# Optimization experiments

Hardware: AMD Instinct MI355X
Metric: run time of the kernel (lower is better)

Reference implementation:

```python
import jax, jax.numpy as jnp
import numpy as np

B, L, HC, D = 4, 4096, 4, 1024
K, DIL = 4, 2
EPS = 1e-5
C = HC * D
PAD = (K - 1) * DIL


def setup_inputs() -> dict:
    key = jax.random.key(0)
    k1, k2, k3 = jax.random.split(key, 3)
    x = jax.random.normal(k1, (B, L, HC, D), dtype=jnp.float32)
    # RMSNorm affine weights, one per chunk (torch init: ones; randomize slightly for a
    # non-trivial baseline)
    norm_weight = 1.0 + 0.02 * jax.random.normal(k2, (HC, D), dtype=jnp.float32)
    # depthwise conv weight [C, 1, K] (torch init is zeros; use small random values so
    # the kernel-correctness baseline is non-degenerate)
    conv_weight = 0.1 * jax.random.normal(k3, (C, 1, K), dtype=jnp.float32)
    return {"x": x, "norm_weight": norm_weight, "conv_weight": conv_weight}


def reference(x, norm_weight, conv_weight):
    # per-chunk RMSNorm over last dim: [B, L, HC, D]
    ms = jnp.mean(jnp.square(x), axis=-1, keepdims=True)
    xn = x * jax.lax.rsqrt(ms + EPS) * norm_weight[None, None, :, :]
    # concat chunks along feature dim -> [B, L, C], then to [B, C, L]
    xc = xn.reshape(B, L, C).transpose(0, 2, 1)
    # depthwise dilated causal conv1d: left-pad (K-1)*DIL, output length L
    y = jax.lax.conv_general_dilated(
        xc, conv_weight,
        window_strides=(1,),
        padding=((PAD, 0),),
        rhs_dilation=(DIL,),
        feature_group_count=C,
        dimension_numbers=("NCH", "OIH", "NCH"),
    )
    y = jax.nn.silu(y)
    # back to [B, L, HC, D]
    return y.transpose(0, 2, 1).reshape(B, L, HC, D)
```

## Files before the change

kernel.cpp:

```cpp
#include <hip/hip_runtime.h>

namespace {

constexpr int B = 4, L = 4096, HC = 4, D = 1024, K = 4, DIL = 2;
constexpr int PAD = (K - 1) * DIL;
constexpr float EPS = 1e-5f;
constexpr int CL = 64;
constexpr int ST = 8;
constexpr int NSTEP = CL / ST;
constexpr int NT = L / CL;
constexpr int BDIM = 256;

typedef float f32x4 __attribute__((ext_vector_type(4)));

#define LGKM_BARRIER() do {                                    \
    asm volatile("s_waitcnt lgkmcnt(0)" ::: "memory");         \
    __builtin_amdgcn_s_barrier();                              \
} while (0)

__device__ __forceinline__ void stage16(const float* g, float* l) {
    __builtin_amdgcn_global_load_lds(
        (const __attribute__((address_space(1))) void*)g,
        (__attribute__((address_space(3))) void*)l, 16, 0, 0);
}

__global__ __launch_bounds__(BDIM, 2) void engram_shortconv_ldspipe(
    const float* __restrict__ x,
    const float* __restrict__ nw,
    const float* __restrict__ cw,
    float* __restrict__ out)
{
    __shared__ float s_buf[2][ST][BDIM * 4];
    __shared__ float s_part[ST][BDIM];
    __shared__ float s_inv[ST];

    const int blk = blockIdx.x;
    const int t   = blk % NT;
    const int hc  = (blk / NT) % HC;
    const int b   = blk / (NT * HC);
    const int l0  = t * CL;

    const int tid  = threadIdx.x;
    const int wave = tid >> 6;
    const int lane = tid & 63;

    const size_t rs = (size_t)HC * D;
    const float* xcol = x   + ((size_t)b * L * HC + (size_t)hc) * D + tid * 4;
    float*       ocol = out + ((size_t)b * L * HC + (size_t)hc) * D + tid * 4;

    const float4 nw4 = *(const float4*)(nw + (size_t)hc * D + tid * 4);
    float4 cwv[4];
    #pragma unroll
    for (int j = 0; j < 4; ++j)
        cwv[j] = *(const float4*)(cw + ((size_t)hc * D + tid * 4 + j) * K);

    float win[PAD][4];
    if (l0 >= PAD) {
        #pragma unroll
        for (int r = 0; r < PAD; ++r) {
            const float4 v = *(const float4*)(xcol + (size_t)(l0 - PAD + r) * rs);
            win[r][0] = v.x; win[r][1] = v.y; win[r][2] = v.z; win[r][3] = v.w;
        }
    } else {
        #pragma unroll
        for (int r = 0; r < PAD; ++r) {
            const int l = l0 - PAD + r;
            float4 v = make_float4(0.f, 0.f, 0.f, 0.f);
            if (l >= 0) v = *(const float4*)(xcol + (size_t)l * rs);
            win[r][0] = v.x; win[r][1] = v.y; win[r][2] = v.z; win[r][3] = v.w;
        }
    }

    #pragma unroll
    for (int r = 0; r < ST; ++r)
        stage16(xcol + (size_t)(l0 + r) * rs, &s_buf[0][r][wave * 256]);
    #pragma unroll
    for (int r = 0; r < ST; ++r)
        stage16(xcol + (size_t)(l0 + ST + r) * rs, &s_buf[1][r][wave * 256]);

    float wk[4][4];
    {
        const float gv[4] = { nw4.x, nw4.y, nw4.z, nw4.w };
        #pragma unroll
        for (int j = 0; j < 4; ++j) {
            wk[j][0] = cwv[j].x * gv[j]; wk[j][1] = cwv[j].y * gv[j];
            wk[j][2] = cwv[j].z * gv[j]; wk[j][3] = cwv[j].w * gv[j];
        }
    }

    #pragma unroll
    for (int r = 0; r < PAD; ++r)
        s_part[r][tid] = win[r][0]*win[r][0] + win[r][1]*win[r][1]
                       + win[r][2]*win[r][2] + win[r][3]*win[r][3];
    LGKM_BARRIER();
    {
        int rr = wave;
        float s1 = s_part[rr][lane]       + s_part[rr][lane + 64]
                 + s_part[rr][lane + 128] + s_part[rr][lane + 192];
        #pragma unroll
        for (int off = 32; off >= 1; off >>= 1) s1 += __shfl_xor(s1, off);
        if (lane == 0) s_inv[rr] = rsqrtf(s1 * (1.0f / D) + EPS);
        rr = wave + 4;
        if (rr < PAD) {
            float s2 = s_part[rr][lane]       + s_part[rr][lane + 64]
                     + s_part[rr][lane + 128] + s_part[rr][lane + 192];
            #pragma unroll
            for (int off = 32; off >= 1; off >>= 1) s2 += __shfl_xor(s2, off);
            if (lane == 0) s_inv[rr] = rsqrtf(s2 * (1.0f / D) + EPS);
        }
    }
    LGKM_BARRIER();
    #pragma unroll
    for (int r = 0; r < PAD; ++r) {
        const float iv = s_inv[r];
        win[r][0] *= iv; win[r][1] *= iv; win[r][2] *= iv; win[r][3] *= iv;
    }

    #pragma unroll
    for (int s = 0; s < NSTEP; ++s) {
        const int cb = s & 1;

        if (s == 0)                 asm volatile("s_waitcnt vmcnt(8)"  ::: "memory");
        else if (s == 1)            asm volatile("s_waitcnt vmcnt(16)" ::: "memory");
        else if (s == NSTEP - 1)    asm volatile("s_waitcnt vmcnt(16)" ::: "memory");
        else                        asm volatile("s_waitcnt vmcnt(24)" ::: "memory");
        __builtin_amdgcn_sched_barrier(0);

        float cur[ST][4];
        #pragma unroll
        for (int r = 0; r < ST; ++r) {
            const f32x4 v = *(const f32x4*)&s_buf[cb][r][tid * 4];
            cur[r][0] = v.x; cur[r][1] = v.y; cur[r][2] = v.z; cur[r][3] = v.w;
        }
        #pragma unroll
        for (int r = 0; r < ST; ++r)
            s_part[r][tid] = cur[r][0]*cur[r][0] + cur[r][1]*cur[r][1]
                           + cur[r][2]*cur[r][2] + cur[r][3]*cur[r][3];

        if (s < NSTEP - 2) {
            asm volatile("s_waitcnt lgkmcnt(0)" ::: "memory");
            __builtin_amdgcn_sched_barrier(0);
            #pragma unroll
            for (int r = 0; r < ST; ++r)
                stage16(xcol + (size_t)(l0 + (s + 2) * ST + r) * rs,
                        &s_buf[cb][r][wave * 256]);
            __builtin_amdgcn_sched_barrier(0);
        }

        LGKM_BARRIER();
        {
            int rr = wave;
            float s1 = s_part[rr][lane]       + s_part[rr][lane + 64]
                     + s_part[rr][lane + 128] + s_part[rr][lane + 192];
            #pragma unroll
            for (int off = 32; off >= 1; off >>= 1) s1 += __shfl_xor(s1, off);
            if (lane == 0) s_inv[rr] = rsqrtf(s1 * (1.0f / D) + EPS);
            rr = wave + 4;
            float s2 = s_part[rr][lane]       + s_part[rr][lane + 64]
                     + s_part[rr][lane + 128] + s_part[rr][lane + 192];
            #pragma unroll
            for (int off = 32; off >= 1; off >>= 1) s2 += __shfl_xor(s2, off);
            if (lane == 0) s_inv[rr] = rsqrtf(s2 * (1.0f / D) + EPS);
        }
        LGKM_BARRIER();

        const int base = l0 + s * ST;
        #pragma unroll
        for (int r = 0; r < ST; ++r) {
            const float iv = s_inv[r];
            cur[r][0] *= iv; cur[r][1] *= iv; cur[r][2] *= iv; cur[r][3] *= iv;
        }

        #pragma unroll
        for (int i = 0; i < ST; ++i) {
            float av[4];
            #pragma unroll
            for (int j = 0; j < 4; ++j) {
                float a = 0.0f;
                #pragma unroll
                for (int k = 0; k < 4; ++k) {
                    const int rel = i - 6 + 2 * k;
                    const float xv = (rel < 0) ? win[6 + rel][j] : cur[rel][j];
                    a = fmaf(wk[j][k], xv, a);
                }
                av[j] = a / (1.0f + __expf(-a));
            }
            f32x4 o = { av[0], av[1], av[2], av[3] };
            *(f32x4*)(ocol + (size_t)(base + i) * rs) = o;
        }

        #pragma unroll
        for (int r = 0; r < PAD; ++r) {
            win[r][0] = cur[r + 2][0]; win[r][1] = cur[r + 2][1];
            win[r][2] = cur[r + 2][2]; win[r][3] = cur[r + 2][3];
        }
    }
}

}

extern "C" void kernel_launch(void* const* d_in, const int* in_sizes, int n_in,
                              void* d_out, int out_size, void* d_ws, size_t ws_size,
                              hipStream_t stream) {
    const float* x  = (const float*)d_in[0];
    const float* nw = (const float*)d_in[1];
    const float* cw = (const float*)d_in[2];
    float* out = (float*)d_out;

    const int nblocks = B * HC * NT;
    engram_shortconv_ldspipe<<<dim3(nblocks), dim3(BDIM), 0, stream>>>(x, nw, cw, out);
}
```

Measured before the change: 111.7 us.

## Triple-buffer LDS staging and compute row norms one step ahead

Switches from a double-buffered 8-row stage to a triple-buffered 4-row stage pipeline. Each wave now computes one row's RMS directly from LDS one step ahead, which removes the s_part partial-sum buffer and one barrier per step. The halo rows' norms are computed from global loads, and occupancy is raised to 4 blocks per CU. The blockIdx is also remapped to interleave tiles across XCDs. The cost is more loop iterations and more prefetch bookkeeping, with tighter vmcnt waits.

Result: no change. 111.8 us (+0.1%).

```diff
diff --git a/kernel.cpp b/kernel.cpp
--- a/kernel.cpp
+++ b/kernel.cpp
@@ -2,12 +2,12 @@
 
 namespace {
 
-constexpr int B = 4, L = 4096, HC = 4, D = 1024, K = 4, DIL = 2;
-constexpr int PAD = (K - 1) * DIL;
+constexpr int NB = 4, L = 4096, HC = 4, D = 1024, KW = 4;
+constexpr int PAD = 6;
 constexpr float EPS = 1e-5f;
-constexpr int CL = 64;
-constexpr int ST = 8;
-constexpr int NSTEP = CL / ST;
+constexpr int ST = 4;
+constexpr int NSTEP = 16;
+constexpr int CL = ST * NSTEP;
 constexpr int NT = L / CL;
 constexpr int BDIM = 256;
 
@@ -24,59 +24,68 @@
         (__attribute__((address_space(3))) void*)l, 16, 0, 0);
 }
 
-__global__ __launch_bounds__(BDIM, 2) void engram_shortconv_ldspipe(
+__global__ __launch_bounds__(BDIM, 4) void engram_shortconv_tri(
     const float* __restrict__ x,
     const float* __restrict__ nw,
     const float* __restrict__ cw,
     float* __restrict__ out)
 {
-    __shared__ float s_buf[2][ST][BDIM * 4];
-    __shared__ float s_part[ST][BDIM];
-    __shared__ float s_inv[ST];
-
-    const int blk = blockIdx.x;
-    const int t   = blk % NT;
-    const int hc  = (blk / NT) % HC;
-    const int b   = blk / (NT * HC);
-    const int l0  = t * CL;
+    __shared__ float s_buf[3][ST][D];
+    __shared__ float s_inv[2][ST];
+    __shared__ float s_invh[PAD];
+
+    const int lblk = (blockIdx.x & 7) * 128 + (blockIdx.x >> 3);
+    const int t    = lblk % NT;
+    const int hc   = (lblk / NT) % HC;
+    const int b    = lblk / (NT * HC);
+    const int l0   = t * CL;
 
     const int tid  = threadIdx.x;
     const int wave = tid >> 6;
     const int lane = tid & 63;
 
     const size_t rs = (size_t)HC * D;
-    const float* xcol = x   + ((size_t)b * L * HC + (size_t)hc) * D + tid * 4;
-    float*       ocol = out + ((size_t)b * L * HC + (size_t)hc) * D + tid * 4;
+    const float* xbase = x + ((size_t)b * L * HC + (size_t)hc) * D;
+    const float* xcol  = xbase + tid * 4;
+    float*       ocol  = out + ((size_t)b * L * HC + (size_t)hc) * D + tid * 4;
+
+    #pragma unroll
+    for (int s = 0; s < 3; ++s)
+        #pragma unroll
+        for (int r = 0; r < ST; ++r)
+            stage16(xcol + (size_t)(l0 + s * ST + r) * rs, &s_buf[s][r][wave * 256]);
 
     const float4 nw4 = *(const float4*)(nw + (size_t)hc * D + tid * 4);
     float4 cwv[4];
     #pragma unroll
     for (int j = 0; j < 4; ++j)
-        cwv[j] = *(const float4*)(cw + ((size_t)hc * D + tid * 4 + j) * K);
+        cwv[j] = *(const float4*)(cw + ((size_t)hc * D + tid * 4 + j) * KW);
 
     float win[PAD][4];
-    if (l0 >= PAD) {
-        #pragma unroll
-        for (int r = 0; r < PAD; ++r) {
-            const float4 v = *(const float4*)(xcol + (size_t)(l0 - PAD + r) * rs);
-            win[r][0] = v.x; win[r][1] = v.y; win[r][2] = v.z; win[r][3] = v.w;
-        }
-    } else {
-        #pragma unroll
-        for (int r = 0; r < PAD; ++r) {
-            const int l = l0 - PAD + r;
-            float4 v = make_float4(0.f, 0.f, 0.f, 0.f);
-            if (l >= 0) v = *(const float4*)(xcol + (size_t)l * rs);
-            win[r][0] = v.x; win[r][1] = v.y; win[r][2] = v.z; win[r][3] = v.w;
-        }
-    }
-
-    #pragma unroll
-    for (int r = 0; r < ST; ++r)
-        stage16(xcol + (size_t)(l0 + r) * rs, &s_buf[0][r][wave * 256]);
-    #pragma unroll
-    for (int r = 0; r < ST; ++r)
-        stage16(xcol + (size_t)(l0 + ST + r) * rs, &s_buf[1][r][wave * 256]);
+    #pragma unroll
+    for (int r = 0; r < PAD; ++r) {
+        const int l = l0 - PAD + r;
+        float4 v = make_float4(0.f, 0.f, 0.f, 0.f);
+        if (l >= 0) v = *(const float4*)(xcol + (size_t)l * rs);
+        win[r][0] = v.x; win[r][1] = v.y; win[r][2] = v.z; win[r][3] = v.w;
+    }
+
+    #pragma unroll
+    for (int rr = wave; rr < PAD; rr += 4) {
+        const int l = l0 - PAD + rr;
+        float ss = 0.0f;
+        if (l >= 0) {
+            const float* rp = xbase + (size_t)l * rs;
+            #pragma unroll
+            for (int q = 0; q < 4; ++q) {
+                const f32x4 v = *(const f32x4*)(rp + lane * 4 + q * 256);
+                ss = fmaf(v.x, v.x, fmaf(v.y, v.y, fmaf(v.z, v.z, fmaf(v.w, v.w, ss))));
+            }
+        }
+        #pragma unroll
+        for (int off = 32; off >= 1; off >>= 1) ss += __shfl_xor(ss, off);
+        if (lane == 0) s_invh[rr] = rsqrtf(ss * (1.0f / D) + EPS);
+    }
 
     float wk[4][4];
     {
@@ -88,89 +97,53 @@
         }
     }
 
-    #pragma unroll
-    for (int r = 0; r < PAD; ++r)
-        s_part[r][tid] = win[r][0]*win[r][0] + win[r][1]*win[r][1]
-                       + win[r][2]*win[r][2] + win[r][3]*win[r][3];
     LGKM_BARRIER();
+    #pragma unroll
+    for (int r = 0; r < PAD; ++r) {
+        const float iv = s_invh[r];
+        win[r][0] *= iv; win[r][1] *= iv; win[r][2] *= iv; win[r][3] *= iv;
+    }
+    asm volatile("s_waitcnt vmcnt(0)" ::: "memory");
+    __builtin_amdgcn_s_barrier();
     {
-        int rr = wave;
-        float s1 = s_part[rr][lane]       + s_part[rr][lane + 64]
-                 + s_part[rr][lane + 128] + s_part[rr][lane + 192];
-        #pragma unroll
-        for (int off = 32; off >= 1; off >>= 1) s1 += __shfl_xor(s1, off);
-        if (lane == 0) s_inv[rr] = rsqrtf(s1 * (1.0f / D) + EPS);
-        rr = wave + 4;
-        if (rr < PAD) {
-            float s2 = s_part[rr][lane]       + s_part[rr][lane + 64]
-                     + s_part[rr][lane + 128] + s_part[rr][lane + 192];
-            #pragma unroll
-            for (int off = 32; off >= 1; off >>= 1) s2 += __shfl_xor(s2, off);
-            if (lane == 0) s_inv[rr] = rsqrtf(s2 * (1.0f / D) + EPS);
-        }
+        const int row = wave;
+        float ss = 0.0f;
+        #pragma unroll
+        for (int q = 0; q < 4; ++q) {
+            const f32x4 v = *(const f32x4*)&s_buf[0][row][lane * 4 + q * 256];
+            ss = fmaf(v.x, v.x, fmaf(v.y, v.y, fmaf(v.z, v.z, fmaf(v.w, v.w, ss))));
+        }
+        #pragma unroll
+        for (int off = 32; off >= 1; off >>= 1) ss += __shfl_xor(ss, off);
+        if (lane == 0) s_inv[0][row] = rsqrtf(ss * (1.0f / D) + EPS);
     }
     LGKM_BARRIER();
-    #pragma unroll
-    for (int r = 0; r < PAD; ++r) {
-        const float iv = s_inv[r];
-        win[r][0] *= iv; win[r][1] *= iv; win[r][2] *= iv; win[r][3] *= iv;
-    }
 
     #pragma unroll
     for (int s = 0; s < NSTEP; ++s) {
-        const int cb = s & 1;
-
-        if (s == 0)                 asm volatile("s_waitcnt vmcnt(8)"  ::: "memory");
-        else if (s == 1)            asm volatile("s_waitcnt vmcnt(16)" ::: "memory");
-        else if (s == NSTEP - 1)    asm volatile("s_waitcnt vmcnt(16)" ::: "memory");
-        else                        asm volatile("s_waitcnt vmcnt(24)" ::: "memory");
-        __builtin_amdgcn_sched_barrier(0);
-
+        if (s < NSTEP - 1) {
+            const int row = wave;
+            const float* rp = &s_buf[(s + 1) % 3][row][0];
+            float ss = 0.0f;
+            #pragma unroll
+            for (int q = 0; q < 4; ++q) {
+                const f32x4 v = *(const f32x4*)(rp + lane * 4 + q * 256);
+                ss = fmaf(v.x, v.x, fmaf(v.y, v.y, fmaf(v.z, v.z, fmaf(v.w, v.w, ss))));
+            }
+            #pragma unroll
+            for (int off = 32; off >= 1; off >>= 1) ss += __shfl_xor(ss, off);
+            if (lane == 0) s_inv[(s + 1) & 1][row] = rsqrtf(ss * (1.0f / D) + EPS);
+        }
+
+        const int base = l0 + s * ST;
         float cur[ST][4];
         #pragma unroll
         for (int r = 0; r < ST; ++r) {
-            const f32x4 v = *(const f32x4*)&s_buf[cb][r][tid * 4];
-            cur[r][0] = v.x; cur[r][1] = v.y; cur[r][2] = v.z; cur[r][3] = v.w;
-        }
-        #pragma unroll
-        for (int r = 0; r < ST; ++r)
-            s_part[r][tid] = cur[r][0]*cur[r][0] + cur[r][1]*cur[r][1]
-                           + cur[r][2]*cur[r][2] + cur[r][3]*cur[r][3];
-
-        if (s < NSTEP - 2) {
-            asm volatile("s_waitcnt lgkmcnt(0)" ::: "memory");
-            __builtin_amdgcn_sched_barrier(0);
-            #pragma unroll
-            for (int r = 0; r < ST; ++r)
-                stage16(xcol + (size_t)(l0 + (s + 2) * ST + r) * rs,
-                        &s_buf[cb][r][wave * 256]);
-            __builtin_amdgcn_sched_barrier(0);
-        }
-
-        LGKM_BARRIER();
-        {
-            int rr = wave;
-            float s1 = s_part[rr][lane]       + s_part[rr][lane + 64]
-                     + s_part[rr][lane + 128] + s_part[rr][lane + 192];
-            #pragma unroll
-            for (int off = 32; off >= 1; off >>= 1) s1 += __shfl_xor(s1, off);
-            if (lane == 0) s_inv[rr] = rsqrtf(s1 * (1.0f / D) + EPS);
-            rr = wave + 4;
-            float s2 = s_part[rr][lane]       + s_part[rr][lane + 64]
-                     + s_part[rr][lane + 128] + s_part[rr][lane + 192];
-            #pragma unroll
-            for (int off = 32; off >= 1; off >>= 1) s2 += __shfl_xor(s2, off);
-            if (lane == 0) s_inv[rr] = rsqrtf(s2 * (1.0f / D) + EPS);
-        }
-        LGKM_BARRIER();
-
-        const int base = l0 + s * ST;
-        #pragma unroll
-        for (int r = 0; r < ST; ++r) {
-            const float iv = s_inv[r];
-            cur[r][0] *= iv; cur[r][1] *= iv; cur[r][2] *= iv; cur[r][3] *= iv;
-        }
-
+            const f32x4 v = *(const f32x4*)&s_buf[s % 3][r][tid * 4];
+            const float iv = s_inv[s & 1][r];
+            cur[r][0] = v.x * iv; cur[r][1] = v.y * iv;
+            cur[r][2] = v.z * iv; cur[r][3] = v.w * iv;
+        }
         #pragma unroll
         for (int i = 0; i < ST; ++i) {
             float av[4];
@@ -189,11 +162,27 @@
             *(f32x4*)(ocol + (size_t)(base + i) * rs) = o;
         }
 
-        #pragma unroll
-        for (int r = 0; r < PAD; ++r) {
-            win[r][0] = cur[r + 2][0]; win[r][1] = cur[r + 2][1];
-            win[r][2] = cur[r + 2][2]; win[r][3] = cur[r + 2][3];
-        }
+        win[0][0]=win[4][0]; win[0][1]=win[4][1]; win[0][2]=win[4][2]; win[0][3]=win[4][3];
+        win[1][0]=win[5][0]; win[1][1]=win[5][1]; win[1][2]=win[5][2]; win[1][3]=win[5][3];
+        #pragma unroll
+        for (int r = 0; r < ST; ++r) {
+            win[2 + r][0] = cur[r][0]; win[2 + r][1] = cur[r][1];
+            win[2 + r][2] = cur[r][2]; win[2 + r][3] = cur[r][3];
+        }
+
+        if (s < NSTEP - 3) {
+            asm volatile("s_waitcnt lgkmcnt(0)" ::: "memory");
+            __builtin_amdgcn_sched_barrier(0);
+            #pragma unroll
+            for (int r = 0; r < ST; ++r)
+                stage16(xcol + (size_t)(l0 + (s + 3) * ST + r) * rs,
+                        &s_buf[s % 3][r][wave * 256]);
+            __builtin_amdgcn_sched_barrier(0);
+        }
+
+        if (s <= NSTEP - 4)      asm volatile("s_waitcnt vmcnt(8)" ::: "memory");
+        else if (s == NSTEP - 3) asm volatile("s_waitcnt vmcnt(4)" ::: "memory");
+        if (s < NSTEP - 1) LGKM_BARRIER();
     }
 }
 
@@ -207,6 +196,6 @@
     const float* cw = (const float*)d_in[2];
     float* out = (float*)d_out;
 
-    const int nblocks = B * HC * NT;
-    engram_shortconv_ldspipe<<<dim3(nblocks), dim3(BDIM), 0, stream>>>(x, nw, cw, out);
-}
+    const int nblocks = NB * HC * NT;
+    engram_shortconv_tri<<<dim3(nblocks), dim3(BDIM), 0, stream>>>(x, nw, cw, out);
+}
```
